# Kernel tuning notes

Hardware: AMD Instinct MI355X
Metric: run time of the kernel (lower is better)

The kernel has to match this reference:

```python
import jax, jax.numpy as jnp
import numpy as np

EMBED_DIM = 1024
NUM_HEADS = 16
HEAD_DIM = EMBED_DIM // NUM_HEADS


def setup_inputs() -> dict:
    key = jax.random.key(0)
    ks = jax.random.split(key, 6)
    s = 1.0 / np.sqrt(EMBED_DIM)
    x = jax.random.normal(ks[0], (2, 2048, EMBED_DIM), dtype=jnp.float32)
    Wk = jax.random.uniform(ks[1], (EMBED_DIM, EMBED_DIM), jnp.float32, -s, s)
    Wq = jax.random.uniform(ks[2], (EMBED_DIM, EMBED_DIM), jnp.float32, -s, s)
    Wv = jax.random.uniform(ks[3], (EMBED_DIM, EMBED_DIM), jnp.float32, -s, s)
    Wo = jax.random.uniform(ks[4], (EMBED_DIM, EMBED_DIM), jnp.float32, -s, s)
    bo = jax.random.uniform(ks[5], (EMBED_DIM,), jnp.float32, -s, s)
    return {"x": x, "Wq": Wq, "Wk": Wk, "Wv": Wv, "Wo": Wo, "bo": bo}


def reference(x, Wq, Wk, Wv, Wo, bo):
    b, s, e = x.shape
    h, d = NUM_HEADS, HEAD_DIM
    scale = d ** (-0.5)
    # nn.Linear: y = x @ W.T ; here W stored as [out, in] -> use W.T
    q = (x @ Wq.T).reshape(b, s, h, d).transpose(0, 2, 1, 3)  # b h s d
    k = (x @ Wk.T).reshape(b, s, h, d).transpose(0, 2, 1, 3)
    v = (x @ Wv.T).reshape(b, s, h, d).transpose(0, 2, 1, 3)
    logits = jnp.einsum('bhqd,bhkd->bhqk', q, k) * scale
    attn = jax.nn.softmax(logits, axis=-1)
    out = jnp.einsum('bhqk,bhkd->bhqd', attn, v)
    out = out.transpose(0, 2, 1, 3).reshape(b, s, e)
    return out @ Wo.T + bo
```

## Files before the change

kernel.cpp:

```cpp
#include <hip/hip_runtime.h>
#include <hip/hip_bf16.h>

using short8 = __attribute__((ext_vector_type(8))) short;
using f32x4  = __attribute__((ext_vector_type(4))) float;

#if __has_builtin(__builtin_amdgcn_exp2f)
#define EXP2(x) __builtin_amdgcn_exp2f(x)
#else
#define EXP2(x) exp2f(x)
#endif

__device__ __forceinline__ short f2bf(float f) {
    union { float f; unsigned u; } v; v.f = f;
    unsigned r = v.u + 0x7fffu + ((v.u >> 16) & 1u);
    return (short)(r >> 16);
}
__device__ __forceinline__ unsigned pack_trunc(float a, float b) {
    union { float f; unsigned u; } ua, ub; ua.f = a; ub.f = b;
#if __has_builtin(__builtin_amdgcn_perm)
    return __builtin_amdgcn_perm(ub.u, ua.u, 0x07060302u);
#else
    return (ub.u & 0xFFFF0000u) | (ua.u >> 16);
#endif
}
__device__ __forceinline__ void async_copy16(const short* g, short* s) {
    __builtin_amdgcn_global_load_lds(
        (const __attribute__((address_space(1))) void*)g,
        (__attribute__((address_space(3))) void*)s, 16, 0, 0);
}

__global__ __launch_bounds__(256) void cvt_f32_bf16(
    const float* __restrict__ s0, const float* __restrict__ s1,
    const float* __restrict__ s2, const float* __restrict__ s3,
    const float* __restrict__ s4,
    short* __restrict__ d0, short* __restrict__ d1, short* __restrict__ d2,
    short* __restrict__ d3, short* __restrict__ d4,
    int n0, int n1, int n2, int n3, int n4) {
    const float* s; short* d; int n;
    switch (blockIdx.y) {
        case 0: s = s0; d = d0; n = n0; break;
        case 1: s = s1; d = d1; n = n1; break;
        case 2: s = s2; d = d2; n = n2; break;
        case 3: s = s3; d = d3; n = n3; break;
        default: s = s4; d = d4; n = n4; break;
    }
    const int idx = (blockIdx.x * 256 + threadIdx.x) * 4;
    if (idx < n) {
        float4 v = *(const float4*)(s + idx);
        short4 o;
        o.x = f2bf(v.x); o.y = f2bf(v.y); o.z = f2bf(v.z); o.w = f2bf(v.w);
        *(short4*)(d + idx) = o;
    }
}

template <int MODE>
__device__ __forceinline__ void gemm_body(const short* __restrict__ A,
                                          const short* __restrict__ B,
                                          short* __restrict__ C,
                                          float scale) {
    constexpr int Kd = 1024, Nd = 1024, Sd = 2048;
    __shared__ __align__(16) short As[128 * 32];
    __shared__ __align__(16) short Bs[128 * 32];

    const int tid  = threadIdx.x;
    const int w    = tid >> 6, lane = tid & 63;
    const int quad = lane >> 4, l16 = lane & 15;
    const int wm   = (w >> 1) * 64, wn = (w & 1) * 64;
    const int bm   = blockIdx.y * 128, bn = blockIdx.x * 128;

    f32x4 acc[4][4];
#pragma unroll
    for (int i = 0; i < 4; ++i)
#pragma unroll
        for (int j = 0; j < 4; ++j) acc[i][j] = (f32x4){0.f, 0.f, 0.f, 0.f};

    for (int k0 = 0; k0 < Kd; k0 += 32) {
        __syncthreads();
#pragma unroll
        for (int c = 0; c < 2; ++c) {
            int li  = c * 256 + tid;
            int row = li >> 2;
            int col = (li & 3) * 8;
            async_copy16(A + (size_t)(bm + row) * Kd + k0 + col, &As[li * 8]);
            async_copy16(B + (size_t)(bn + row) * Kd + k0 + col, &Bs[li * 8]);
        }
        __syncthreads();

        short8 af[4], bfv[4];
#pragma unroll
        for (int mi = 0; mi < 4; ++mi)
            af[mi] = *(const short8*)(&As[(wm + mi * 16 + l16) * 32 + quad * 8]);
#pragma unroll
        for (int ni = 0; ni < 4; ++ni)
            bfv[ni] = *(const short8*)(&Bs[(wn + ni * 16 + l16) * 32 + quad * 8]);
#pragma unroll
        for (int mi = 0; mi < 4; ++mi)
#pragma unroll
            for (int ni = 0; ni < 4; ++ni) {
                if constexpr (MODE == 2)
                    acc[mi][ni] = __builtin_amdgcn_mfma_f32_16x16x32_bf16(
                        bfv[ni], af[mi], acc[mi][ni], 0, 0, 0);
                else
                    acc[mi][ni] = __builtin_amdgcn_mfma_f32_16x16x32_bf16(
                        af[mi], bfv[ni], acc[mi][ni], 0, 0, 0);
            }
    }

    if constexpr (MODE == 2) {
#pragma unroll
        for (int mi = 0; mi < 4; ++mi) {
            const int m_g = bm + wm + mi * 16 + l16;
            const int b_  = m_g >> 11, s_ = m_g & 2047;
#pragma unroll
            for (int ni = 0; ni < 4; ++ni)
#pragma unroll
                for (int r = 0; r < 4; ++r) {
                    const int n_g = bn + wn + ni * 16 + quad * 4 + r;
                    C[(size_t)b_ * Nd * Sd + (size_t)n_g * Sd + s_] =
                        f2bf(acc[mi][ni][r]);
                }
        }
    } else {
#pragma unroll
        for (int ni = 0; ni < 4; ++ni) {
            const int colg = bn + wn + ni * 16 + l16;
#pragma unroll
            for (int mi = 0; mi < 4; ++mi)
#pragma unroll
                for (int r = 0; r < 4; ++r) {
                    const int rowg = bm + wm + mi * 16 + quad * 4 + r;
                    C[(size_t)rowg * Nd + colg] = f2bf(acc[mi][ni][r] * scale);
                }
        }
    }
}

#define CSC 0.18033688f

__global__ __launch_bounds__(256, 2) void proj_gemm(
    const short* __restrict__ X,
    const short* __restrict__ Wq, const short* __restrict__ Wk,
    const short* __restrict__ Wv,
    short* __restrict__ Qo, short* __restrict__ Ko, short* __restrict__ VTo) {
    if (blockIdx.z == 0)
        gemm_body<0>(X, Wq, Qo, CSC);
    else if (blockIdx.z == 1)
        gemm_body<0>(X, Wk, Ko, 1.0f);
    else
        gemm_body<2>(X, Wv, VTo, 1.0f);
}

__global__ __launch_bounds__(256, 2) void out_gemm(
    const short* __restrict__ A, const short* __restrict__ B,
    const float* __restrict__ bias, float* __restrict__ C) {
    constexpr int Kd = 1024, Nd = 1024;
    __shared__ __align__(16) short As[128 * 32];
    __shared__ __align__(16) short Bs[64 * 32];

    const int tid  = threadIdx.x;
    const int w    = tid >> 6, lane = tid & 63;
    const int quad = lane >> 4, l16 = lane & 15;
    const int wm   = (w >> 1) * 64, wn = (w & 1) * 32;
    const int bm   = blockIdx.y * 128, bn = blockIdx.x * 64;

    f32x4 acc[4][2];
#pragma unroll
    for (int i = 0; i < 4; ++i)
#pragma unroll
        for (int j = 0; j < 2; ++j) acc[i][j] = (f32x4){0.f, 0.f, 0.f, 0.f};

    for (int k0 = 0; k0 < Kd; k0 += 32) {
        __syncthreads();
#pragma unroll
        for (int c = 0; c < 2; ++c) {
            int li  = c * 256 + tid;
            int row = li >> 2;
            int col = (li & 3) * 8;
            async_copy16(A + (size_t)(bm + row) * Kd + k0 + col, &As[li * 8]);
        }
        {
            int row = tid >> 2, col = (tid & 3) * 8;
            async_copy16(B + (size_t)(bn + row) * Kd + k0 + col, &Bs[tid * 8]);
        }
        __syncthreads();

        short8 af[4], bfv[2];
#pragma unroll
        for (int mi = 0; mi < 4; ++mi)
            af[mi] = *(const short8*)(&As[(wm + mi * 16 + l16) * 32 + quad * 8]);
#pragma unroll
        for (int ni = 0; ni < 2; ++ni)
            bfv[ni] = *(const short8*)(&Bs[(wn + ni * 16 + l16) * 32 + quad * 8]);
#pragma unroll
        for (int mi = 0; mi < 4; ++mi)
#pragma unroll
            for (int ni = 0; ni < 2; ++ni)
                acc[mi][ni] = __builtin_amdgcn_mfma_f32_16x16x32_bf16(
                    af[mi], bfv[ni], acc[mi][ni], 0, 0, 0);
    }

#pragma unroll
    for (int ni = 0; ni < 2; ++ni) {
        const int colg = bn + wn + ni * 16 + l16;
        const float bv = bias[colg];
#pragma unroll
        for (int mi = 0; mi < 4; ++mi)
#pragma unroll
            for (int r = 0; r < 4; ++r) {
                const int rowg = bm + wm + mi * 16 + quad * 4 + r;
                C[(size_t)rowg * Nd + colg] = acc[mi][ni][r] + bv;
            }
    }
}

__global__ __launch_bounds__(256, 2) void attn_kernel(
    const short* __restrict__ Q, const short* __restrict__ K,
    const short* __restrict__ VT, short* __restrict__ O) {
    constexpr int S = 2048, E = 1024;
    __shared__ __align__(16) short Ks[64 * 64];
    __shared__ __align__(16) short Vs[64 * 64];
    __shared__ __align__(16) short Pt[4 * 32 * 72];

    const int tid  = threadIdx.x;
    const int w    = tid >> 6, lane = tid & 63;
    const int quad = lane >> 4, l16 = lane & 15;
    const int bh   = blockIdx.y, b = bh >> 4, h = bh & 15;
    const int qt   = blockIdx.x;

    const int    q0   = qt * 128 + w * 32;
    const size_t base = (size_t)b * S * E;
    const size_t vtb  = (size_t)b * E * S;
    const int    hc   = h * 64;

    short8 aq[2][2];
#pragma unroll
    for (int qg = 0; qg < 2; ++qg) {
        const short* qp = Q + base + (size_t)(q0 + qg * 16 + l16) * E + hc + quad * 8;
        aq[qg][0] = *(const short8*)(qp);
        aq[qg][1] = *(const short8*)(qp + 32);
    }

    f32x4 oT[2][4], o_sum[2];
#pragma unroll
    for (int qg = 0; qg < 2; ++qg) {
        o_sum[qg] = (f32x4){0.f, 0.f, 0.f, 0.f};
#pragma unroll
        for (int i = 0; i < 4; ++i) oT[qg][i] = (f32x4){0.f, 0.f, 0.f, 0.f};
    }

    int          sdst[2];
    const short* kga[2];
    const short* vga[2];
#pragma unroll
    for (int c = 0; c < 2; ++c) {
        int li = c * 256 + tid, row = li >> 3, cc = li & 7;
        sdst[c] = row * 64 + ((cc ^ (row & 7)) * 8);
        kga[c]  = K + base + (size_t)row * E + hc + cc * 8;
        vga[c]  = VT + vtb + (size_t)(hc + row) * S + cc * 8;
    }

    short8 kr[2], vr[2];
#pragma unroll
    for (int c = 0; c < 2; ++c) {
        kr[c] = *(const short8*)(kga[c]);
        vr[c] = *(const short8*)(vga[c]);
    }

    const short8 ones = (short8){0x3F80, 0x3F80, 0x3F80, 0x3F80,
                                 0x3F80, 0x3F80, 0x3F80, 0x3F80};
    const float  LB   = 0.00281502f;
    short*       Ptw  = &Pt[w * 32 * 72];
    const int    xr   = l16 & 7;

    for (int kt = 0; kt < S / 64; ++kt) {
        __syncthreads();
#pragma unroll
        for (int c = 0; c < 2; ++c) {
            *(short8*)(&Ks[sdst[c]]) = kr[c];
            *(short8*)(&Vs[sdst[c]]) = vr[c];
        }
        __syncthreads();

        if (kt + 1 < S / 64) {
#pragma unroll
            for (int c = 0; c < 2; ++c) {
                kr[c] = *(const short8*)(kga[c] + (size_t)(kt + 1) * 64 * E);
                vr[c] = *(const short8*)(vga[c] + (kt + 1) * 64);
            }
        }

#pragma unroll
        for (int kn = 0; kn < 4; ++kn) {
            const short* kb  = &Ks[(kn * 16 + l16) * 64];
            short8       bk0 = *(const short8*)(kb + ((quad ^ xr) * 8));
            short8       bk1 = *(const short8*)(kb + (((quad + 4) ^ xr) * 8));
#pragma unroll
            for (int qg = 0; qg < 2; ++qg) {
                f32x4 a = (f32x4){LB, LB, LB, LB};
                a = __builtin_amdgcn_mfma_f32_16x16x32_bf16(bk0, aq[qg][0], a, 0, 0, 0);
                a = __builtin_amdgcn_mfma_f32_16x16x32_bf16(bk1, aq[qg][1], a, 0, 0, 0);
                float e0 = EXP2(a[0]), e1 = EXP2(a[1]);
                float e2 = EXP2(a[2]), e3 = EXP2(a[3]);
                uint2 pk;
                pk.x = pack_trunc(e0, e1);
                pk.y = pack_trunc(e2, e3);
                *(uint2*)(&Ptw[(qg * 16 + l16) * 72 + kn * 16 + quad * 4]) = pk;
            }
        }

#pragma unroll
        for (int ks = 0; ks < 2; ++ks) {
            short8 pf[2];
#pragma unroll
            for (int qg = 0; qg < 2; ++qg) {
                pf[qg] = *(const short8*)(
                    &Ptw[(qg * 16 + l16) * 72 + ks * 32 + quad * 8]);
                o_sum[qg] = __builtin_amdgcn_mfma_f32_16x16x32_bf16(
                    ones, pf[qg], o_sum[qg], 0, 0, 0);
            }
#pragma unroll
            for (int ni = 0; ni < 4; ++ni) {
                const int rv = ni * 16 + l16;
                short8 vb =
                    *(const short8*)(&Vs[rv * 64 + (((ks * 4 + quad) ^ (rv & 7)) * 8)]);
#pragma unroll
                for (int qg = 0; qg < 2; ++qg)
                    oT[qg][ni] = __builtin_amdgcn_mfma_f32_16x16x32_bf16(
                        vb, pf[qg], oT[qg][ni], 0, 0, 0);
            }
        }
    }

#pragma unroll
    for (int qg = 0; qg < 2; ++qg) {
        const float inv = 1.0f / o_sum[qg][0];
        const int   qg_ = q0 + qg * 16 + l16;
#pragma unroll
        for (int ni = 0; ni < 4; ++ni) {
            short4 ov;
            ov.x = f2bf(oT[qg][ni][0] * inv);
            ov.y = f2bf(oT[qg][ni][1] * inv);
            ov.z = f2bf(oT[qg][ni][2] * inv);
            ov.w = f2bf(oT[qg][ni][3] * inv);
            *(short4*)(&O[base + (size_t)qg_ * E + hc + ni * 16 + quad * 4]) = ov;
        }
    }
}

extern "C" void kernel_launch(void* const* d_in, const int* in_sizes, int n_in,
                              void* d_out, int out_size, void* d_ws, size_t ws_size,
                              hipStream_t stream) {
    const float* x  = (const float*)d_in[0];
    const float* Wq = (const float*)d_in[1];
    const float* Wk = (const float*)d_in[2];
    const float* Wv = (const float*)d_in[3];
    const float* Wo = (const float*)d_in[4];
    const float* bo = (const float*)d_in[5];
    float* out = (float*)d_out;

    constexpr int XN = 2 * 2048 * 1024;
    constexpr int WN = 1024 * 1024;

    short* Xb  = (short*)d_ws;
    short* Wqb = Xb + XN;
    short* Wkb = Wqb + WN;
    short* Wvb = Wkb + WN;
    short* Wob = Wvb + WN;
    short* Qb  = Wob + WN;
    short* Kb  = Qb + XN;
    short* VTb = Kb + XN;

    cvt_f32_bf16<<<dim3(4096, 5), 256, 0, stream>>>(
        x, Wq, Wk, Wv, Wo, Xb, Wqb, Wkb, Wvb, Wob, XN, WN, WN, WN, WN);
    proj_gemm<<<dim3(8, 32, 3), 256, 0, stream>>>(Xb, Wqb, Wkb, Wvb, Qb, Kb, VTb);
    attn_kernel<<<dim3(16, 32), 256, 0, stream>>>(Qb, Kb, VTb, Xb );
    out_gemm<<<dim3(16, 32), 256, 0, stream>>>(Xb, Wob, bo, out);
}
```

Before: 187.3 us.

## Double-buffer attention K/V tiles, keep P in registers, reuse GEMM body for output

```diff
diff --git a/kernel.cpp b/kernel.cpp
--- a/kernel.cpp
+++ b/kernel.cpp
@@ -3,6 +3,7 @@
 
 using short8 = __attribute__((ext_vector_type(8))) short;
 using f32x4  = __attribute__((ext_vector_type(4))) float;
+using uint4v = __attribute__((ext_vector_type(4))) unsigned;
 
 #if __has_builtin(__builtin_amdgcn_exp2f)
 #define EXP2(x) __builtin_amdgcn_exp2f(x)
@@ -53,10 +54,11 @@
     }
 }
 
-template <int MODE>
+template <int MODE, typename OT>
 __device__ __forceinline__ void gemm_body(const short* __restrict__ A,
                                           const short* __restrict__ B,
-                                          short* __restrict__ C,
+                                          OT* __restrict__ C,
+                                          const float* __restrict__ bias,
                                           float scale) {
     constexpr int Kd = 1024, Nd = 1024, Sd = 2048;
     __shared__ __align__(16) short As[128 * 32];
@@ -124,12 +126,16 @@
 #pragma unroll
         for (int ni = 0; ni < 4; ++ni) {
             const int colg = bn + wn + ni * 16 + l16;
+            const float bv = (MODE == 1) ? bias[colg] : 0.f;
 #pragma unroll
             for (int mi = 0; mi < 4; ++mi)
 #pragma unroll
                 for (int r = 0; r < 4; ++r) {
                     const int rowg = bm + wm + mi * 16 + quad * 4 + r;
-                    C[(size_t)rowg * Nd + colg] = f2bf(acc[mi][ni][r] * scale);
+                    if constexpr (MODE == 0)
+                        C[(size_t)rowg * Nd + colg] = f2bf(acc[mi][ni][r] * scale);
+                    else
+                        C[(size_t)rowg * Nd + colg] = acc[mi][ni][r] + bv;
                 }
         }
     }
@@ -143,83 +149,25 @@
     const short* __restrict__ Wv,
     short* __restrict__ Qo, short* __restrict__ Ko, short* __restrict__ VTo) {
     if (blockIdx.z == 0)
-        gemm_body<0>(X, Wq, Qo, CSC);
+        gemm_body<0, short>(X, Wq, Qo, nullptr, CSC);
     else if (blockIdx.z == 1)
-        gemm_body<0>(X, Wk, Ko, 1.0f);
+        gemm_body<0, short>(X, Wk, Ko, nullptr, 1.0f);
     else
-        gemm_body<2>(X, Wv, VTo, 1.0f);
+        gemm_body<2, short>(X, Wv, VTo, nullptr, 1.0f);
 }
 
 __global__ __launch_bounds__(256, 2) void out_gemm(
-    const short* __restrict__ A, const short* __restrict__ B,
+    const short* __restrict__ A, const short* __restrict__ W,
     const float* __restrict__ bias, float* __restrict__ C) {
-    constexpr int Kd = 1024, Nd = 1024;
-    __shared__ __align__(16) short As[128 * 32];
-    __shared__ __align__(16) short Bs[64 * 32];
-
-    const int tid  = threadIdx.x;
-    const int w    = tid >> 6, lane = tid & 63;
-    const int quad = lane >> 4, l16 = lane & 15;
-    const int wm   = (w >> 1) * 64, wn = (w & 1) * 32;
-    const int bm   = blockIdx.y * 128, bn = blockIdx.x * 64;
-
-    f32x4 acc[4][2];
-#pragma unroll
-    for (int i = 0; i < 4; ++i)
-#pragma unroll
-        for (int j = 0; j < 2; ++j) acc[i][j] = (f32x4){0.f, 0.f, 0.f, 0.f};
-
-    for (int k0 = 0; k0 < Kd; k0 += 32) {
-        __syncthreads();
-#pragma unroll
-        for (int c = 0; c < 2; ++c) {
-            int li  = c * 256 + tid;
-            int row = li >> 2;
-            int col = (li & 3) * 8;
-            async_copy16(A + (size_t)(bm + row) * Kd + k0 + col, &As[li * 8]);
-        }
-        {
-            int row = tid >> 2, col = (tid & 3) * 8;
-            async_copy16(B + (size_t)(bn + row) * Kd + k0 + col, &Bs[tid * 8]);
-        }
-        __syncthreads();
-
-        short8 af[4], bfv[2];
-#pragma unroll
-        for (int mi = 0; mi < 4; ++mi)
-            af[mi] = *(const short8*)(&As[(wm + mi * 16 + l16) * 32 + quad * 8]);
-#pragma unroll
-        for (int ni = 0; ni < 2; ++ni)
-            bfv[ni] = *(const short8*)(&Bs[(wn + ni * 16 + l16) * 32 + quad * 8]);
-#pragma unroll
-        for (int mi = 0; mi < 4; ++mi)
-#pragma unroll
-            for (int ni = 0; ni < 2; ++ni)
-                acc[mi][ni] = __builtin_amdgcn_mfma_f32_16x16x32_bf16(
-                    af[mi], bfv[ni], acc[mi][ni], 0, 0, 0);
-    }
-
-#pragma unroll
-    for (int ni = 0; ni < 2; ++ni) {
-        const int colg = bn + wn + ni * 16 + l16;
-        const float bv = bias[colg];
-#pragma unroll
-        for (int mi = 0; mi < 4; ++mi)
-#pragma unroll
-            for (int r = 0; r < 4; ++r) {
-                const int rowg = bm + wm + mi * 16 + quad * 4 + r;
-                C[(size_t)rowg * Nd + colg] = acc[mi][ni][r] + bv;
-            }
-    }
+    gemm_body<1, float>(A, W, C, bias, 1.0f);
 }
 
 __global__ __launch_bounds__(256, 2) void attn_kernel(
     const short* __restrict__ Q, const short* __restrict__ K,
     const short* __restrict__ VT, short* __restrict__ O) {
-    constexpr int S = 2048, E = 1024;
-    __shared__ __align__(16) short Ks[64 * 64];
-    __shared__ __align__(16) short Vs[64 * 64];
-    __shared__ __align__(16) short Pt[4 * 32 * 72];
+    constexpr int S = 2048, E = 1024, NT = S / 64;
+    __shared__ __align__(16) short Ks[2][64 * 64];
+    __shared__ __align__(16) short Vs[2][64 * 64];
 
     const int tid  = threadIdx.x;
     const int w    = tid >> 6, lane = tid & 63;
@@ -231,6 +179,7 @@
     const size_t base = (size_t)b * S * E;
     const size_t vtb  = (size_t)b * E * S;
     const int    hc   = h * 64;
+    const int    xr   = l16 & 7;
 
     short8 aq[2][2];
 #pragma unroll
@@ -248,15 +197,19 @@
         for (int i = 0; i < 4; ++i) oT[qg][i] = (f32x4){0.f, 0.f, 0.f, 0.f};
     }
 
-    int          sdst[2];
+    int          kdst[2], vdst0[2], vdst1[2];
     const short* kga[2];
     const short* vga[2];
 #pragma unroll
     for (int c = 0; c < 2; ++c) {
         int li = c * 256 + tid, row = li >> 3, cc = li & 7;
-        sdst[c] = row * 64 + ((cc ^ (row & 7)) * 8);
-        kga[c]  = K + base + (size_t)row * E + hc + cc * 8;
-        vga[c]  = VT + vtb + (size_t)(hc + row) * S + cc * 8;
+        kdst[c] = row * 64 + ((cc ^ (row & 7)) * 8);
+        int c0   = 4 * (cc >> 2) + 2 * (cc & 1);
+        int boff = 4 * ((cc >> 1) & 1);
+        vdst0[c] = row * 64 + ((c0 ^ (row & 7)) * 8) + boff;
+        vdst1[c] = row * 64 + (((c0 + 1) ^ (row & 7)) * 8) + boff;
+        kga[c]   = K + base + (size_t)row * E + hc + cc * 8;
+        vga[c]   = VT + vtb + (size_t)(hc + row) * S + cc * 8;
     }
 
     short8 kr[2], vr[2];
@@ -265,33 +218,56 @@
         kr[c] = *(const short8*)(kga[c]);
         vr[c] = *(const short8*)(vga[c]);
     }
+#pragma unroll
+    for (int c = 0; c < 2; ++c) {
+        *(short8*)(&Ks[0][kdst[c]]) = kr[c];
+        short4 lo, hi;
+        lo.x = vr[c][0]; lo.y = vr[c][1]; lo.z = vr[c][2]; lo.w = vr[c][3];
+        hi.x = vr[c][4]; hi.y = vr[c][5]; hi.z = vr[c][6]; hi.w = vr[c][7];
+        *(short4*)(&Vs[0][vdst0[c]]) = lo;
+        *(short4*)(&Vs[0][vdst1[c]]) = hi;
+    }
+#pragma unroll
+    for (int c = 0; c < 2; ++c) {
+        kr[c] = *(const short8*)(kga[c] + (size_t)64 * E);
+        vr[c] = *(const short8*)(vga[c] + 64);
+    }
+    __syncthreads();
 
     const short8 ones = (short8){0x3F80, 0x3F80, 0x3F80, 0x3F80,
                                  0x3F80, 0x3F80, 0x3F80, 0x3F80};
     const float  LB   = 0.00281502f;
-    short*       Ptw  = &Pt[w * 32 * 72];
-    const int    xr   = l16 & 7;
-
-    for (int kt = 0; kt < S / 64; ++kt) {
-        __syncthreads();
-#pragma unroll
-        for (int c = 0; c < 2; ++c) {
-            *(short8*)(&Ks[sdst[c]]) = kr[c];
-            *(short8*)(&Vs[sdst[c]]) = vr[c];
-        }
-        __syncthreads();
-
-        if (kt + 1 < S / 64) {
+
+    for (int kt = 0; kt < NT; ++kt) {
+        const int    cur = kt & 1;
+        const short* Kc  = Ks[cur];
+        const short* Vc  = Vs[cur];
+
+        if (kt + 1 < NT) {
+            short* Kn = Ks[cur ^ 1];
+            short* Vn = Vs[cur ^ 1];
 #pragma unroll
             for (int c = 0; c < 2; ++c) {
-                kr[c] = *(const short8*)(kga[c] + (size_t)(kt + 1) * 64 * E);
-                vr[c] = *(const short8*)(vga[c] + (kt + 1) * 64);
-            }
-        }
-
+                *(short8*)(&Kn[kdst[c]]) = kr[c];
+                short4 lo, hi;
+                lo.x = vr[c][0]; lo.y = vr[c][1]; lo.z = vr[c][2]; lo.w = vr[c][3];
+                hi.x = vr[c][4]; hi.y = vr[c][5]; hi.z = vr[c][6]; hi.w = vr[c][7];
+                *(short4*)(&Vn[vdst0[c]]) = lo;
+                *(short4*)(&Vn[vdst1[c]]) = hi;
+            }
+            if (kt + 2 < NT) {
+#pragma unroll
+                for (int c = 0; c < 2; ++c) {
+                    kr[c] = *(const short8*)(kga[c] + (size_t)(kt + 2) * 64 * E);
+                    vr[c] = *(const short8*)(vga[c] + (kt + 2) * 64);
+                }
+            }
+        }
+
+        uint4v pkv[2][2];
 #pragma unroll
         for (int kn = 0; kn < 4; ++kn) {
-            const short* kb  = &Ks[(kn * 16 + l16) * 64];
+            const short* kb  = &Kc[(kn * 16 + l16) * 64];
             short8       bk0 = *(const short8*)(kb + ((quad ^ xr) * 8));
             short8       bk1 = *(const short8*)(kb + (((quad + 4) ^ xr) * 8));
 #pragma unroll
@@ -299,12 +275,8 @@
                 f32x4 a = (f32x4){LB, LB, LB, LB};
                 a = __builtin_amdgcn_mfma_f32_16x16x32_bf16(bk0, aq[qg][0], a, 0, 0, 0);
                 a = __builtin_amdgcn_mfma_f32_16x16x32_bf16(bk1, aq[qg][1], a, 0, 0, 0);
-                float e0 = EXP2(a[0]), e1 = EXP2(a[1]);
-                float e2 = EXP2(a[2]), e3 = EXP2(a[3]);
-                uint2 pk;
-                pk.x = pack_trunc(e0, e1);
-                pk.y = pack_trunc(e2, e3);
-                *(uint2*)(&Ptw[(qg * 16 + l16) * 72 + kn * 16 + quad * 4]) = pk;
+                pkv[qg][kn >> 1][(kn & 1) * 2]     = pack_trunc(EXP2(a[0]), EXP2(a[1]));
+                pkv[qg][kn >> 1][(kn & 1) * 2 + 1] = pack_trunc(EXP2(a[2]), EXP2(a[3]));
             }
         }
 
@@ -313,8 +285,9 @@
             short8 pf[2];
 #pragma unroll
             for (int qg = 0; qg < 2; ++qg) {
-                pf[qg] = *(const short8*)(
-                    &Ptw[(qg * 16 + l16) * 72 + ks * 32 + quad * 8]);
+                union { uint4v u; short8 s; } cv;
+                cv.u   = pkv[qg][ks];
+                pf[qg] = cv.s;
                 o_sum[qg] = __builtin_amdgcn_mfma_f32_16x16x32_bf16(
                     ones, pf[qg], o_sum[qg], 0, 0, 0);
             }
@@ -322,13 +295,14 @@
             for (int ni = 0; ni < 4; ++ni) {
                 const int rv = ni * 16 + l16;
                 short8 vb =
-                    *(const short8*)(&Vs[rv * 64 + (((ks * 4 + quad) ^ (rv & 7)) * 8)]);
+                    *(const short8*)(&Vc[rv * 64 + (((ks * 4 + quad) ^ xr) * 8)]);
 #pragma unroll
                 for (int qg = 0; qg < 2; ++qg)
                     oT[qg][ni] = __builtin_amdgcn_mfma_f32_16x16x32_bf16(
                         vb, pf[qg], oT[qg][ni], 0, 0, 0);
             }
         }
+        __syncthreads();
     }
 
 #pragma unroll
@@ -374,5 +348,5 @@
         x, Wq, Wk, Wv, Wo, Xb, Wqb, Wkb, Wvb, Wob, XN, WN, WN, WN, WN);
     proj_gemm<<<dim3(8, 32, 3), 256, 0, stream>>>(Xb, Wqb, Wkb, Wvb, Qb, Kb, VTb);
     attn_kernel<<<dim3(16, 32), 256, 0, stream>>>(Qb, Kb, VTb, Xb );
-    out_gemm<<<dim3(16, 32), 256, 0, stream>>>(Xb, Wob, bo, out);
-}
+    out_gemm<<<dim3(8, 32, 1), 256, 0, stream>>>(Xb, Wob, bo, out);
+}
```

After: 178.9 us. 1.05x faster.
